# Kernel optimization log

Hardware: AMD Instinct MI355X
Metric: run time of the kernel (lower is better)

Reference implementation:

```python
import jax, jax.numpy as jnp
import numpy as np

INPUT_SIZE = 1024
HIDDEN_SIZE = 1024
BATCH = 8192


def setup_inputs() -> dict:
    key = jax.random.key(0)
    ks = jax.random.split(key, 10)
    H, I, B = HIDDEN_SIZE, INPUT_SIZE, BATCH
    s = 1.0 / np.sqrt(H)  # scale params so activations stay in sane range
    return {
        "input": jax.random.normal(ks[0], (B, I), jnp.float32),
        "hx": jax.random.normal(ks[1], (B, H), jnp.float32),
        "cx": jax.random.normal(ks[2], (B, H), jnp.float32),
        "att": jax.random.normal(ks[3], (B, I), jnp.float32),
        "weight_ih": jax.random.normal(ks[4], (4 * H, I), jnp.float32) * s,
        "weight_hh": jax.random.normal(ks[5], (4 * H, H), jnp.float32) * s,
        "bias_ih": jax.random.normal(ks[6], (4 * H,), jnp.float32),
        "bias_hh": jax.random.normal(ks[7], (4 * H,), jnp.float32),
        "weight_att": jax.random.normal(ks[8], (2 * H, I), jnp.float32) * s,
        "bias_att": jax.random.normal(ks[9], (2 * H,), jnp.float32),
    }


def reference(input, hx, cx, att, weight_ih, weight_hh, bias_ih, bias_hh,
              weight_att, bias_att):
    H = weight_hh.shape[1]
    # gates: [B, 4H]
    gates = input @ weight_ih.T + bias_ih + hx @ weight_hh.T + bias_hh
    att_gates = att @ weight_att.T + bias_att  # [B, 2H]
    ingate, forgetgate, cellgate, outgate = jnp.split(gates, 4, axis=1)
    ingate_att, attgate = jnp.split(att_gates, 2, axis=1)
    ingate = jax.nn.sigmoid(ingate)
    forgetgate = jax.nn.sigmoid(forgetgate)
    cellgate = jnp.tanh(cellgate)
    ingate_att = jax.nn.sigmoid(ingate_att)
    attgate = jnp.tanh(attgate)
    outgate = jax.nn.sigmoid(outgate)
    cy = forgetgate * cx + ingate * cellgate + ingate_att * attgate
    hy = outgate * jnp.tanh(cy)
    return (hy, cy)
```

## Files before the change

kernel.cpp:

```cpp
#include <hip/hip_runtime.h>


typedef __attribute__((ext_vector_type(8))) __bf16 bf16x8;
typedef __attribute__((ext_vector_type(8))) unsigned short ushort8;
typedef __attribute__((ext_vector_type(4))) float f32x4;

#define AS1 __attribute__((address_space(1)))
#define AS3 __attribute__((address_space(3)))

__device__ __forceinline__ void gld16(const unsigned short* g, unsigned short* l) {
    __builtin_amdgcn_global_load_lds((const AS1 void*)g, (AS3 void*)l, 16, 0, 0);
}

__device__ __forceinline__ unsigned short f2bf(float f) {
    unsigned int u = __builtin_bit_cast(unsigned int, f);
    u += 0x7fffu + ((u >> 16) & 1u);
    return (unsigned short)(u >> 16);
}

__device__ __forceinline__ float sigmoidf_(float x) { return 1.f / (1.f + __expf(-x)); }
__device__ __forceinline__ float tanhf_(float x) {
    float e = __expf(-2.f * fabsf(x));
    float t = (1.f - e) / (1.f + e);
    return x >= 0.f ? t : -t;
}

__device__ __forceinline__ bf16x8 ldfrag(const unsigned short* p) {
    return __builtin_bit_cast(bf16x8, *(const ushort8*)p);
}

__global__ void cast_bf16_k(unsigned short* __restrict__ dst, const float* __restrict__ src,
                            int n4, int dst_ld, int dst_off) {
    int i = blockIdx.x * blockDim.x + threadIdx.x;
    if (i >= n4) return;
    int e = i * 4;
    int r = e >> 10;
    int c = e & 1023;
    const float4 v = *(const float4*)(src + e);
    ushort4 p;
    p.x = f2bf(v.x); p.y = f2bf(v.y); p.z = f2bf(v.z); p.w = f2bf(v.w);
    *(ushort4*)(dst + r * dst_ld + dst_off + c) = p;
}

__global__ void bias_sum_k(float* __restrict__ dst, const float* __restrict__ a,
                           const float* __restrict__ b, int n) {
    int i = blockIdx.x * blockDim.x + threadIdx.x;
    if (i < n) dst[i] = a[i] + b[i];
}

__global__ __launch_bounds__(256, 2) void att_gemm_k(
    const unsigned short* __restrict__ ATT, const unsigned short* __restrict__ WA,
    const float* __restrict__ bias_att, float* __restrict__ attprod)
{
    __shared__ unsigned short As[128 * 32];
    __shared__ unsigned short Bs[128 * 32];
    const int tid  = threadIdx.x;
    const int wave = tid >> 6, lane = tid & 63;
    const int l15 = lane & 15, quad = lane >> 4;
    const int row0 = blockIdx.x * 128;
    const int n0   = blockIdx.y * 64;

    f32x4 acc[2][8];
    const f32x4 z = {0.f, 0.f, 0.f, 0.f};
#pragma unroll
    for (int i = 0; i < 2; ++i)
#pragma unroll
        for (int j = 0; j < 8; ++j) acc[i][j] = z;

    const int ar = tid >> 2, kp = tid & 3;
    const unsigned short* aG0 = ATT + (row0 + ar) * 1024 + kp * 8;
    const unsigned short* aG1 = aG0 + 64 * 1024;
    const unsigned short* bG0 = WA + (n0 + ar) * 1024 + kp * 8;
    const unsigned short* bG1 = WA + (1024 + n0 + ar) * 1024 + kp * 8;
    unsigned short* aL0 = As + tid * 8;  unsigned short* aL1 = As + (tid + 256) * 8;
    unsigned short* bL0 = Bs + tid * 8;  unsigned short* bL1 = Bs + (tid + 256) * 8;

    const int aoff0 = (wave * 32 + l15) * 32 + quad * 8;
    const int aoff1 = aoff0 + 16 * 32;

    for (int kt = 0; kt < 32; ++kt) {
        gld16(aG0, aL0); gld16(aG1, aL1);
        gld16(bG0, bL0); gld16(bG1, bL1);
        aG0 += 32; aG1 += 32; bG0 += 32; bG1 += 32;
        __syncthreads();
        bf16x8 a0 = ldfrag(As + aoff0);
        bf16x8 a1 = ldfrag(As + aoff1);
#pragma unroll
        for (int cf = 0; cf < 8; ++cf) {
            bf16x8 b = ldfrag(Bs + (cf * 16 + l15) * 32 + quad * 8);
            acc[0][cf] = __builtin_amdgcn_mfma_f32_16x16x32_bf16(a0, b, acc[0][cf], 0, 0, 0);
            acc[1][cf] = __builtin_amdgcn_mfma_f32_16x16x32_bf16(a1, b, acc[1][cf], 0, 0, 0);
        }
        __syncthreads();
    }

    const int Rbase = row0 + wave * 32 + quad * 4;
#pragma unroll
    for (int rf = 0; rf < 2; ++rf)
#pragma unroll
        for (int jf = 0; jf < 4; ++jf) {
            int col = n0 + jf * 16 + l15;
            float b0 = bias_att[col], b1 = bias_att[1024 + col];
#pragma unroll
            for (int reg = 0; reg < 4; ++reg) {
                int R = Rbase + rf * 16 + reg;
                float ia = sigmoidf_(acc[rf][jf][reg] + b0);
                float ag = tanhf_(acc[rf][4 + jf][reg] + b1);
                attprod[R * 1024 + col] = ia * ag;
            }
        }
}

__global__ __launch_bounds__(256, 2) void main_gemm_k(
    const unsigned short* __restrict__ XH, const unsigned short* __restrict__ W4,
    const float* __restrict__ bias4, const float* __restrict__ attprod,
    const float* __restrict__ cx, float* __restrict__ out)
{
    __shared__ unsigned short As[128 * 32];
    __shared__ unsigned short Bs[128 * 32];
    const int tid  = threadIdx.x;
    const int wave = tid >> 6, lane = tid & 63;
    const int l15 = lane & 15, quad = lane >> 4;
    const int row0 = blockIdx.x * 128;
    const int n0   = blockIdx.y * 32;

    f32x4 acc[2][8];
    const f32x4 z = {0.f, 0.f, 0.f, 0.f};
#pragma unroll
    for (int i = 0; i < 2; ++i)
#pragma unroll
        for (int j = 0; j < 8; ++j) acc[i][j] = z;

    const int ar = tid >> 2, kp = tid & 3;
    const unsigned short* aG0 = XH + (row0 + ar) * 2048 + kp * 8;
    const unsigned short* aG1 = aG0 + 64 * 2048;
    const unsigned short* bG0 = W4 + ((ar >> 5) * 1024 + n0 + (ar & 31)) * 2048 + kp * 8;
    const unsigned short* bG1 = bG0 + 2 * 1024 * 2048;
    unsigned short* aL0 = As + tid * 8;  unsigned short* aL1 = As + (tid + 256) * 8;
    unsigned short* bL0 = Bs + tid * 8;  unsigned short* bL1 = Bs + (tid + 256) * 8;

    const int aoff0 = (wave * 32 + l15) * 32 + quad * 8;
    const int aoff1 = aoff0 + 16 * 32;

    for (int kt = 0; kt < 64; ++kt) {
        gld16(aG0, aL0); gld16(aG1, aL1);
        gld16(bG0, bL0); gld16(bG1, bL1);
        aG0 += 32; aG1 += 32; bG0 += 32; bG1 += 32;
        __syncthreads();
        bf16x8 a0 = ldfrag(As + aoff0);
        bf16x8 a1 = ldfrag(As + aoff1);
#pragma unroll
        for (int cf = 0; cf < 8; ++cf) {
            bf16x8 b = ldfrag(Bs + (cf * 16 + l15) * 32 + quad * 8);
            acc[0][cf] = __builtin_amdgcn_mfma_f32_16x16x32_bf16(a0, b, acc[0][cf], 0, 0, 0);
            acc[1][cf] = __builtin_amdgcn_mfma_f32_16x16x32_bf16(a1, b, acc[1][cf], 0, 0, 0);
        }
        __syncthreads();
    }

    const int Rbase = row0 + wave * 32 + quad * 4;
    const int CYOFF = 8192 * 1024;
#pragma unroll
    for (int rf = 0; rf < 2; ++rf)
#pragma unroll
        for (int jp = 0; jp < 2; ++jp) {
            int col = n0 + jp * 16 + l15;
            float bi = bias4[col];
            float bff = bias4[1024 + col];
            float bg = bias4[2048 + col];
            float bo = bias4[3072 + col];
#pragma unroll
            for (int reg = 0; reg < 4; ++reg) {
                int R = Rbase + rf * 16 + reg;
                int off = R * 1024 + col;
                float ig = sigmoidf_(acc[rf][0 + jp][reg] + bi);
                float fg = sigmoidf_(acc[rf][2 + jp][reg] + bff);
                float gg = tanhf_(acc[rf][4 + jp][reg] + bg);
                float og = sigmoidf_(acc[rf][6 + jp][reg] + bo);
                float cyv = fg * cx[off] + ig * gg + attprod[off];
                float hyv = og * tanhf_(cyv);
                out[off] = hyv;
                out[CYOFF + off] = cyv;
            }
        }
}

extern "C" void kernel_launch(void* const* d_in, const int* in_sizes, int n_in,
                              void* d_out, int out_size, void* d_ws, size_t ws_size,
                              hipStream_t stream) {
    const float* input = (const float*)d_in[0];
    const float* hx    = (const float*)d_in[1];
    const float* cx    = (const float*)d_in[2];
    const float* att   = (const float*)d_in[3];
    const float* w_ih  = (const float*)d_in[4];
    const float* w_hh  = (const float*)d_in[5];
    const float* b_ih  = (const float*)d_in[6];
    const float* b_hh  = (const float*)d_in[7];
    const float* w_att = (const float*)d_in[8];
    const float* b_att = (const float*)d_in[9];
    float* out = (float*)d_out;

    char* ws = (char*)d_ws;
    unsigned short* XH   = (unsigned short*)(ws);
    unsigned short* ATTb = (unsigned short*)(ws + 33554432);
    unsigned short* W4   = (unsigned short*)(ws + 50331648);
    unsigned short* WA   = (unsigned short*)(ws + 67108864);
    float* bias4         = (float*)(ws + 71303168);
    float* attprod       = (float*)(ws + 71319552);

    const int blk = 256;
    auto g4 = [](int n) { return (n / 4 + 255) / 256; };
    cast_bf16_k<<<g4(8192 * 1024), blk, 0, stream>>>(XH, input, 8192 * 1024 / 4, 2048, 0);
    cast_bf16_k<<<g4(8192 * 1024), blk, 0, stream>>>(XH, hx,    8192 * 1024 / 4, 2048, 1024);
    cast_bf16_k<<<g4(8192 * 1024), blk, 0, stream>>>(ATTb, att, 8192 * 1024 / 4, 1024, 0);
    cast_bf16_k<<<g4(4096 * 1024), blk, 0, stream>>>(W4, w_ih,  4096 * 1024 / 4, 2048, 0);
    cast_bf16_k<<<g4(4096 * 1024), blk, 0, stream>>>(W4, w_hh,  4096 * 1024 / 4, 2048, 1024);
    cast_bf16_k<<<g4(2048 * 1024), blk, 0, stream>>>(WA, w_att, 2048 * 1024 / 4, 1024, 0);
    bias_sum_k<<<16, 256, 0, stream>>>(bias4, b_ih, b_hh, 4096);

    att_gemm_k<<<dim3(64, 16), 256, 0, stream>>>(ATTb, WA, b_att, attprod);
    main_gemm_k<<<dim3(64, 32), 256, 0, stream>>>(XH, W4, bias4, attprod, cx, out);
}
```

Before: 452.0 us.

## Swizzle LDS tile layout and fuse all cast kernels into one launch

Both GEMM kernels now XOR-swizzle the 16-byte k-chunk position inside each LDS row, on the global source side and in the fragment read offsets. The goal is to cut LDS bank conflicts when MFMA fragments are read. Separately, the six bf16 cast kernels and the bias-sum kernel are merged into one grid-stride launch, which removes per-launch overhead. The swizzle has to stay consistent between the global_load_lds write pattern and the reads, and a mismatch would silently corrupt results.

```diff
diff --git a/kernel.cpp b/kernel.cpp
--- a/kernel.cpp
+++ b/kernel.cpp
@@ -29,23 +29,32 @@
     return __builtin_bit_cast(bf16x8, *(const ushort8*)p);
 }
 
-__global__ void cast_bf16_k(unsigned short* __restrict__ dst, const float* __restrict__ src,
-                            int n4, int dst_ld, int dst_off) {
-    int i = blockIdx.x * blockDim.x + threadIdx.x;
-    if (i >= n4) return;
-    int e = i * 4;
-    int r = e >> 10;
-    int c = e & 1023;
-    const float4 v = *(const float4*)(src + e);
-    ushort4 p;
-    p.x = f2bf(v.x); p.y = f2bf(v.y); p.z = f2bf(v.z); p.w = f2bf(v.w);
-    *(ushort4*)(dst + r * dst_ld + dst_off + c) = p;
-}
-
-__global__ void bias_sum_k(float* __restrict__ dst, const float* __restrict__ a,
-                           const float* __restrict__ b, int n) {
-    int i = blockIdx.x * blockDim.x + threadIdx.x;
-    if (i < n) dst[i] = a[i] + b[i];
+__global__ void cast_all_k(const float* __restrict__ input, const float* __restrict__ hx,
+                           const float* __restrict__ att,   const float* __restrict__ w_ih,
+                           const float* __restrict__ w_hh,  const float* __restrict__ w_att,
+                           const float* __restrict__ b_ih,  const float* __restrict__ b_hh,
+                           unsigned short* __restrict__ XH, unsigned short* __restrict__ ATTb,
+                           unsigned short* __restrict__ W4, unsigned short* __restrict__ WA,
+                           float* __restrict__ bias4)
+{
+    int gid = blockIdx.x * blockDim.x + threadIdx.x;
+    if (gid < 4096) bias4[gid] = b_ih[gid] + b_hh[gid];
+    const int total = 8912896;
+    for (int i = gid; i < total; i += gridDim.x * blockDim.x) {
+        const float* src; unsigned short* dst; int ld, off, rel;
+        if (i < 2097152)      { src = input; dst = XH;   ld = 2048; off = 0;    rel = i; }
+        else if (i < 4194304) { src = hx;    dst = XH;   ld = 2048; off = 1024; rel = i - 2097152; }
+        else if (i < 6291456) { src = att;   dst = ATTb; ld = 1024; off = 0;    rel = i - 4194304; }
+        else if (i < 7340032) { src = w_ih;  dst = W4;   ld = 2048; off = 0;    rel = i - 6291456; }
+        else if (i < 8388608) { src = w_hh;  dst = W4;   ld = 2048; off = 1024; rel = i - 7340032; }
+        else                  { src = w_att; dst = WA;   ld = 1024; off = 0;    rel = i - 8388608; }
+        int e = rel * 4;
+        int r = e >> 10, c = e & 1023;
+        const float4 v = *(const float4*)(src + e);
+        ushort4 p;
+        p.x = f2bf(v.x); p.y = f2bf(v.y); p.z = f2bf(v.z); p.w = f2bf(v.w);
+        *(ushort4*)(dst + r * ld + off + c) = p;
+    }
 }
 
 __global__ __launch_bounds__(256, 2) void att_gemm_k(
@@ -67,15 +76,17 @@
 #pragma unroll
         for (int j = 0; j < 8; ++j) acc[i][j] = z;
 
-    const int ar = tid >> 2, kp = tid & 3;
-    const unsigned short* aG0 = ATT + (row0 + ar) * 1024 + kp * 8;
+    const int ar = tid >> 2;
+    const int kp_sw = (tid & 3) ^ ((ar >> 1) & 3);
+    const unsigned short* aG0 = ATT + (row0 + ar) * 1024 + kp_sw * 8;
     const unsigned short* aG1 = aG0 + 64 * 1024;
-    const unsigned short* bG0 = WA + (n0 + ar) * 1024 + kp * 8;
-    const unsigned short* bG1 = WA + (1024 + n0 + ar) * 1024 + kp * 8;
+    const unsigned short* bG0 = WA + (n0 + ar) * 1024 + kp_sw * 8;
+    const unsigned short* bG1 = WA + (1024 + n0 + ar) * 1024 + kp_sw * 8;
     unsigned short* aL0 = As + tid * 8;  unsigned short* aL1 = As + (tid + 256) * 8;
     unsigned short* bL0 = Bs + tid * 8;  unsigned short* bL1 = Bs + (tid + 256) * 8;
 
-    const int aoff0 = (wave * 32 + l15) * 32 + quad * 8;
+    const int sw8 = (quad ^ ((l15 >> 1) & 3)) * 8;
+    const int aoff0 = (wave * 32 + l15) * 32 + sw8;
     const int aoff1 = aoff0 + 16 * 32;
 
     for (int kt = 0; kt < 32; ++kt) {
@@ -87,7 +98,7 @@
         bf16x8 a1 = ldfrag(As + aoff1);
 #pragma unroll
         for (int cf = 0; cf < 8; ++cf) {
-            bf16x8 b = ldfrag(Bs + (cf * 16 + l15) * 32 + quad * 8);
+            bf16x8 b = ldfrag(Bs + (cf * 16 + l15) * 32 + sw8);
             acc[0][cf] = __builtin_amdgcn_mfma_f32_16x16x32_bf16(a0, b, acc[0][cf], 0, 0, 0);
             acc[1][cf] = __builtin_amdgcn_mfma_f32_16x16x32_bf16(a1, b, acc[1][cf], 0, 0, 0);
         }
@@ -131,15 +142,17 @@
 #pragma unroll
         for (int j = 0; j < 8; ++j) acc[i][j] = z;
 
-    const int ar = tid >> 2, kp = tid & 3;
-    const unsigned short* aG0 = XH + (row0 + ar) * 2048 + kp * 8;
+    const int ar = tid >> 2;
+    const int kp_sw = (tid & 3) ^ ((ar >> 1) & 3);
+    const unsigned short* aG0 = XH + (row0 + ar) * 2048 + kp_sw * 8;
     const unsigned short* aG1 = aG0 + 64 * 2048;
-    const unsigned short* bG0 = W4 + ((ar >> 5) * 1024 + n0 + (ar & 31)) * 2048 + kp * 8;
+    const unsigned short* bG0 = W4 + ((ar >> 5) * 1024 + n0 + (ar & 31)) * 2048 + kp_sw * 8;
     const unsigned short* bG1 = bG0 + 2 * 1024 * 2048;
     unsigned short* aL0 = As + tid * 8;  unsigned short* aL1 = As + (tid + 256) * 8;
     unsigned short* bL0 = Bs + tid * 8;  unsigned short* bL1 = Bs + (tid + 256) * 8;
 
-    const int aoff0 = (wave * 32 + l15) * 32 + quad * 8;
+    const int sw8 = (quad ^ ((l15 >> 1) & 3)) * 8;
+    const int aoff0 = (wave * 32 + l15) * 32 + sw8;
     const int aoff1 = aoff0 + 16 * 32;
 
     for (int kt = 0; kt < 64; ++kt) {
@@ -151,7 +164,7 @@
         bf16x8 a1 = ldfrag(As + aoff1);
 #pragma unroll
         for (int cf = 0; cf < 8; ++cf) {
-            bf16x8 b = ldfrag(Bs + (cf * 16 + l15) * 32 + quad * 8);
+            bf16x8 b = ldfrag(Bs + (cf * 16 + l15) * 32 + sw8);
             acc[0][cf] = __builtin_amdgcn_mfma_f32_16x16x32_bf16(a0, b, acc[0][cf], 0, 0, 0);
             acc[1][cf] = __builtin_amdgcn_mfma_f32_16x16x32_bf16(a1, b, acc[1][cf], 0, 0, 0);
         }
@@ -165,10 +178,10 @@
 #pragma unroll
         for (int jp = 0; jp < 2; ++jp) {
             int col = n0 + jp * 16 + l15;
-            float bi = bias4[col];
+            float bi  = bias4[col];
             float bff = bias4[1024 + col];
-            float bg = bias4[2048 + col];
-            float bo = bias4[3072 + col];
+            float bg  = bias4[2048 + col];
+            float bo  = bias4[3072 + col];
 #pragma unroll
             for (int reg = 0; reg < 4; ++reg) {
                 int R = Rbase + rf * 16 + reg;
@@ -208,16 +221,8 @@
     float* bias4         = (float*)(ws + 71303168);
     float* attprod       = (float*)(ws + 71319552);
 
-    const int blk = 256;
-    auto g4 = [](int n) { return (n / 4 + 255) / 256; };
-    cast_bf16_k<<<g4(8192 * 1024), blk, 0, stream>>>(XH, input, 8192 * 1024 / 4, 2048, 0);
-    cast_bf16_k<<<g4(8192 * 1024), blk, 0, stream>>>(XH, hx,    8192 * 1024 / 4, 2048, 1024);
-    cast_bf16_k<<<g4(8192 * 1024), blk, 0, stream>>>(ATTb, att, 8192 * 1024 / 4, 1024, 0);
-    cast_bf16_k<<<g4(4096 * 1024), blk, 0, stream>>>(W4, w_ih,  4096 * 1024 / 4, 2048, 0);
-    cast_bf16_k<<<g4(4096 * 1024), blk, 0, stream>>>(W4, w_hh,  4096 * 1024 / 4, 2048, 1024);
-    cast_bf16_k<<<g4(2048 * 1024), blk, 0, stream>>>(WA, w_att, 2048 * 1024 / 4, 1024, 0);
-    bias_sum_k<<<16, 256, 0, stream>>>(bias4, b_ih, b_hh, 4096);
-
+    cast_all_k<<<34816, 256, 0, stream>>>(input, hx, att, w_ih, w_hh, w_att,
+                                          b_ih, b_hh, XH, ATTb, W4, WA, bias4);
     att_gemm_k<<<dim3(64, 16), 256, 0, stream>>>(ATTb, WA, b_att, attprod);
     main_gemm_k<<<dim3(64, 32), 256, 0, stream>>>(XH, W4, bias4, attprod, cx, out);
 }
```

New measurement: 437.6 us. 3.2% less time.
